# Kernel tuning notes

Hardware: AMD Instinct MI355X
Metric: run time of the kernel (lower is better)

Reference implementation:

```python
import jax, jax.numpy as jnp
import numpy as np
from jax import lax


def _lstm_layer(x, h0, c0, W_ih, W_hh, b_ih, b_hh):
    # x: [B,T,I]; precompute input projection for all timesteps: [B,T,4H]
    xg = jnp.einsum('bti,gi->btg', x, W_ih) + b_ih

    def step(carry, xg_t):
        h, c = carry
        gates = xg_t + h @ W_hh.T + b_hh  # [B,4H]
        i, f, g, o = jnp.split(gates, 4, axis=-1)  # PyTorch LSTMCell gate order
        i = jax.nn.sigmoid(i)
        f = jax.nn.sigmoid(f)
        g = jnp.tanh(g)
        o = jax.nn.sigmoid(o)
        c = f * c + i * g
        h = o * jnp.tanh(c)
        return (h, c), h

    (h, c), ys = lax.scan(step, (h0, c0), jnp.swapaxes(xg, 0, 1))  # scan over T
    return jnp.swapaxes(ys, 0, 1), h, c  # [B,T,H], [B,H], [B,H]


def setup_inputs() -> dict:
    key = jax.random.key(0)
    ks = jax.random.split(key, 10)
    B, T, I, H = 128, 256, 256, 1024
    s = 0.02
    return {
        'x': jax.random.normal(ks[0], (B, T, I), jnp.float32),
        'hx0': jnp.zeros((2, B, H), jnp.float32),
        'cx0': jnp.zeros((2, B, H), jnp.float32),
        'W_ih0': jax.random.normal(ks[1], (4 * H, I), jnp.float32) * s,
        'W_hh0': jax.random.normal(ks[2], (4 * H, H), jnp.float32) * s,
        'b_ih0': jax.random.normal(ks[3], (4 * H,), jnp.float32) * s,
        'b_hh0': jax.random.normal(ks[4], (4 * H,), jnp.float32) * s,
        'W_ih1': jax.random.normal(ks[5], (4 * H, H), jnp.float32) * s,
        'W_hh1': jax.random.normal(ks[6], (4 * H, H), jnp.float32) * s,
        'b_ih1': jax.random.normal(ks[7], (4 * H,), jnp.float32) * s,
        'b_hh1': jax.random.normal(ks[8], (4 * H,), jnp.float32) * s,
    }


def reference(x, hx0, cx0, W_ih0, W_hh0, b_ih0, b_hh0, W_ih1, W_hh1, b_ih1, b_hh1):
    # Eval mode / variational_inference=False with dropout=0.0: masks are exact ones.
    x, h, c = _lstm_layer(x, hx0[0], cx0[0], W_ih0, W_hh0, b_ih0, b_hh0)
    x, h, c = _lstm_layer(x, hx0[1], cx0[1], W_ih1, W_hh1, b_ih1, b_hh1)
    return x, h, c
```

## Files before the change

### kernel.cpp

```cpp
#include <hip/hip_runtime.h>

typedef __attribute__((ext_vector_type(8))) short short8;
typedef __attribute__((ext_vector_type(4))) float f32x4;

#define DEV static __device__ __forceinline__

DEV unsigned short f2b(float f) {
    union { float f; unsigned u; } v; v.f = f;
    unsigned r = (v.u + 0x7FFFu + ((v.u >> 16) & 1u)) >> 16;
    return (unsigned short)r;
}
DEV float b2f(unsigned short s) {
    union { unsigned u; float f; } v; v.u = ((unsigned)s) << 16;
    return v.f;
}
DEV float sigm(float x) { return 1.0f / (1.0f + __expf(-x)); }


__global__ void k_f2b(const float* __restrict__ src, unsigned short* __restrict__ dst, int n4) {
    int i = blockIdx.x * blockDim.x + threadIdx.x;
    if (i < n4) {
        float4 v = ((const float4*)src)[i];
        ushort4 o;
        o.x = f2b(v.x); o.y = f2b(v.y); o.z = f2b(v.z); o.w = f2b(v.w);
        ((ushort4*)dst)[i] = o;
    }
}

__global__ void k_perm(const float* __restrict__ src, unsigned short* __restrict__ dst, int Kq) {
    int i = blockIdx.x * blockDim.x + threadIdx.x;
    int total = 4096 * Kq;
    if (i >= total) return;
    int rp = i / Kq, kq = i - rp * Kq;
    int j = rp >> 2, g = rp & 3;
    float4 v = ((const float4*)src)[(size_t)(g * 1024 + j) * Kq + kq];
    ushort4 o;
    o.x = f2b(v.x); o.y = f2b(v.y); o.z = f2b(v.z); o.w = f2b(v.w);
    ((ushort4*)dst)[(size_t)rp * Kq + kq] = o;
}

__global__ void k_bias(const float* __restrict__ bi0, const float* __restrict__ bh0,
                       const float* __restrict__ bi1, const float* __restrict__ bh1,
                       float* __restrict__ d0, float* __restrict__ d1) {
    int i = blockIdx.x * blockDim.x + threadIdx.x;
    if (i < 4096) {
        int j = i >> 2, g = i & 3, s = g * 1024 + j;
        d0[i] = bi0[s] + bh0[s];
        d1[i] = bi1[s] + bh1[s];
    }
}

__global__ void k_init(const float* __restrict__ hx, const float* __restrict__ cx,
                       unsigned* __restrict__ hB0, unsigned* __restrict__ hB1,
                       float* __restrict__ c0, float* __restrict__ c1) {
    int i = blockIdx.x * blockDim.x + threadIdx.x;
    if (i < 128 * 512) {
        int b = i >> 9, j = i & 511;
        const float* p0 = hx + (size_t)b * 1024 + j * 2;
        const float* p1 = hx + 131072 + (size_t)b * 1024 + j * 2;
        hB0[i] = (unsigned)f2b(p0[0]) | ((unsigned)f2b(p0[1]) << 16);
        hB1[i] = (unsigned)f2b(p1[0]) | ((unsigned)f2b(p1[1]) << 16);
        c0[i * 2] = cx[i * 2];
        c0[i * 2 + 1] = cx[i * 2 + 1];
        c1[i * 2] = cx[131072 + i * 2];
        c1[i * 2 + 1] = cx[131072 + i * 2 + 1];
    }
}

__global__ __launch_bounds__(256) void k_gemm(
    const unsigned short* __restrict__ A, const unsigned short* __restrict__ W,
    unsigned short* __restrict__ out, int K, int t0, int TC) {
    __shared__ unsigned short ldsA[128 * 40];
    __shared__ unsigned short ldsB[128 * 40];
    const int tid = threadIdx.x;
    const int w = tid >> 6, l = tid & 63;
    const int wm = w >> 1, wn = w & 1;
    const int bm = blockIdx.x, bn = blockIdx.y;
    const int lr = l & 15, lk = (l >> 4) * 8;

    const int row0 = tid >> 2, inb = (tid & 3) << 4;
    const int row1 = row0 + 64;
    const int v0 = bm * 128 + row0, v1 = bm * 128 + row1;
    const size_t ar0 = (size_t)((v0 / TC) * 256 + t0 + (v0 % TC));
    const size_t ar1 = (size_t)((v1 / TC) * 256 + t0 + (v1 % TC));
    const size_t br0 = (size_t)(bn * 128 + row0);
    const size_t br1 = (size_t)(bn * 128 + row1);

    f32x4 acc[4][4];
#pragma unroll
    for (int a = 0; a < 4; a++)
#pragma unroll
        for (int b = 0; b < 4; b++) acc[a][b] = (f32x4){0.f, 0.f, 0.f, 0.f};

    for (int ks = 0; ks < K; ks += 32) {
        uint4 a0 = *(const uint4*)((const char*)A + (ar0 * K + ks) * 2 + inb);
        uint4 a1 = *(const uint4*)((const char*)A + (ar1 * K + ks) * 2 + inb);
        uint4 b0 = *(const uint4*)((const char*)W + (br0 * K + ks) * 2 + inb);
        uint4 b1 = *(const uint4*)((const char*)W + (br1 * K + ks) * 2 + inb);
        *(uint4*)((char*)ldsA + row0 * 80 + inb) = a0;
        *(uint4*)((char*)ldsA + row1 * 80 + inb) = a1;
        *(uint4*)((char*)ldsB + row0 * 80 + inb) = b0;
        *(uint4*)((char*)ldsB + row1 * 80 + inb) = b1;
        __syncthreads();
        short8 af[4], bf[4];
#pragma unroll
        for (int mt = 0; mt < 4; mt++)
            af[mt] = *(const short8*)((const char*)ldsA + (wm * 64 + mt * 16 + lr) * 80 + lk * 2);
#pragma unroll
        for (int nt = 0; nt < 4; nt++)
            bf[nt] = *(const short8*)((const char*)ldsB + (wn * 64 + nt * 16 + lr) * 80 + lk * 2);
#pragma unroll
        for (int mt = 0; mt < 4; mt++)
#pragma unroll
            for (int nt = 0; nt < 4; nt++)
                acc[mt][nt] = __builtin_amdgcn_mfma_f32_16x16x32_bf16(af[mt], bf[nt], acc[mt][nt], 0, 0, 0);
        __syncthreads();
    }

#pragma unroll
    for (int mt = 0; mt < 4; mt++)
#pragma unroll
        for (int nt = 0; nt < 4; nt++)
#pragma unroll
            for (int v4 = 0; v4 < 4; v4++) {
                int vr = bm * 128 + wm * 64 + mt * 16 + (l >> 4) * 4 + v4;
                int col = bn * 128 + wn * 64 + nt * 16 + lr;
                out[(size_t)vr * 4096 + col] = f2b(acc[mt][nt][v4]);
            }
}

template<int LAYER>
__global__ __launch_bounds__(512, 2) void k_lstm(
    const unsigned short* __restrict__ Wh,
    const unsigned short* __restrict__ xg,
    const float* __restrict__ bias,
    float* __restrict__ cbuf,
    unsigned* __restrict__ hA,
    unsigned* __restrict__ hB,
    unsigned short* __restrict__ y0,
    float* __restrict__ out,
    unsigned* __restrict__ cnt,
    int t0, int TC)
{
    extern __shared__ char smem[];
    unsigned short* ldsW = (unsigned short*)smem;
    float* P0 = (float*)(smem + 64 * 2064);
    float* P1 = P0 + 16 * 132;
    float* P2 = P1 + 16 * 132;

    const int tid = threadIdx.x;
    const int g  = (int)blockIdx.x >> 5;
    const int nb = (int)blockIdx.x & 31;
    const int w  = tid >> 6;
    const int l  = tid & 63;
    const int lr = l & 15, lq = l >> 4;

    {
        const char* src = (const char*)(Wh + (size_t)nb * 128 * 1024);
#pragma unroll
        for (int it = 0; it < 16; it++) {
            int idx = it * 512 + tid;
            int row = idx >> 7, inr = (idx & 127) << 4;
            *(uint4*)(smem + row * 2064 + inr) = *(const uint4*)(src + (size_t)row * 2048 + inr);
        }
    }
    short8 wreg[16];
    {
        const unsigned short* src = Wh + (size_t)(nb * 128 + 64) * 1024 + w * 128;
#pragma unroll
        for (int ct = 0; ct < 4; ct++)
#pragma unroll
            for (int kk = 0; kk < 4; kk++)
                wreg[ct * 4 + kk] =
                    *(const short8*)(src + (size_t)(ct * 16 + lr) * 1024 + kk * 32 + lq * 8);
    }

    const int er = tid >> 4, ep = tid & 15;
    const int eb = g * 16 + (er & 15);
    const int ec0 = nb * 128 + ep * 8;
    const int eu0 = nb * 32 + ep * 2;
    float2 c2 = make_float2(0.f, 0.f);
    float4 bsA = make_float4(0.f, 0.f, 0.f, 0.f);
    float4 bsB = make_float4(0.f, 0.f, 0.f, 0.f);
    if (tid < 256) {
        c2 = *(const float2*)(cbuf + (size_t)eb * 1024 + eu0);
        bsA = *(const float4*)(bias + ec0);
        bsB = *(const float4*)(bias + ec0 + 4);
    }

    const size_t abase = (size_t)(g * 16 + lr) * 256 + (size_t)w * 32 + lq * 2;
    const char* wp = (const char*)ldsW + (size_t)lr * 2064 + w * 256 + lq * 16;

    unsigned* cmy = cnt + g * 32;

    __syncthreads();

    for (int dt = 0; dt < TC; dt++) {
        const int t = t0 + dt;
        uint4 xv = make_uint4(0, 0, 0, 0);
        if (tid < 256)
            xv = *(const uint4*)(xg + (size_t)eb * ((size_t)TC * 4096) + (size_t)dt * 4096 + ec0);

        if (dt > 0) {
            unsigned tgt = 32u * (unsigned)dt;
            while (__hip_atomic_load(cmy, __ATOMIC_RELAXED, __HIP_MEMORY_SCOPE_AGENT) < tgt) {}
        }

        const unsigned long long* ap =
            (const unsigned long long*)((t & 1) ? hA : hB) + abase;
        f32x4 acc[8];
#pragma unroll
        for (int i = 0; i < 8; i++) acc[i] = (f32x4){0.f, 0.f, 0.f, 0.f};
#pragma unroll
        for (int kk = 0; kk < 4; kk++) {
            union { unsigned long long u[2]; short8 s; } av;
            av.u[0] = __hip_atomic_load(ap + kk * 8,     __ATOMIC_RELAXED, __HIP_MEMORY_SCOPE_AGENT);
            av.u[1] = __hip_atomic_load(ap + kk * 8 + 1, __ATOMIC_RELAXED, __HIP_MEMORY_SCOPE_AGENT);
#pragma unroll
            for (int ct = 0; ct < 4; ct++) {
                short8 b = *(const short8*)(wp + (size_t)ct * 16 * 2064 + kk * 64);
                acc[ct] = __builtin_amdgcn_mfma_f32_16x16x32_bf16(av.s, b, acc[ct], 0, 0, 0);
            }
#pragma unroll
            for (int ct = 0; ct < 4; ct++)
                acc[4 + ct] = __builtin_amdgcn_mfma_f32_16x16x32_bf16(av.s, wreg[ct * 4 + kk], acc[4 + ct], 0, 0, 0);
        }

        if (w >= 5) {
            float* P = (w == 5) ? P0 : (w == 6) ? P1 : P2;
#pragma unroll
            for (int i = 0; i < 8; i++)
#pragma unroll
                for (int v = 0; v < 4; v++)
                    P[(lq * 4 + v) * 132 + i * 16 + lr] = acc[i][v];
        }
        __syncthreads();
        if (w >= 2 && w <= 4) {
            float* P = (w == 2) ? P0 : (w == 3) ? P1 : P2;
#pragma unroll
            for (int i = 0; i < 8; i++)
#pragma unroll
                for (int v = 0; v < 4; v++)
                    P[(lq * 4 + v) * 132 + i * 16 + lr] += acc[i][v];
        }
        __syncthreads();
        if (w < 2) {
            float* P = (w == 0) ? P0 : P1;
#pragma unroll
            for (int i = 0; i < 8; i++)
#pragma unroll
                for (int v = 0; v < 4; v++)
                    P[(lq * 4 + v) * 132 + i * 16 + lr] += acc[i][v];
        }
        __syncthreads();

        float h0v = 0.f, h1v = 0.f;
        if (tid < 256) {
            const float* pa = P0 + er * 132 + ep * 8;
            const float* pb = P1 + er * 132 + ep * 8;
            const float* pc = P2 + er * 132 + ep * 8;
            const unsigned short* xs = (const unsigned short*)&xv;
            float p0 = pa[0] + pb[0] + pc[0] + b2f(xs[0]) + bsA.x;
            float p1 = pa[1] + pb[1] + pc[1] + b2f(xs[1]) + bsA.y;
            float p2 = pa[2] + pb[2] + pc[2] + b2f(xs[2]) + bsA.z;
            float p3 = pa[3] + pb[3] + pc[3] + b2f(xs[3]) + bsA.w;
            float q0 = pa[4] + pb[4] + pc[4] + b2f(xs[4]) + bsB.x;
            float q1 = pa[5] + pb[5] + pc[5] + b2f(xs[5]) + bsB.y;
            float q2 = pa[6] + pb[6] + pc[6] + b2f(xs[6]) + bsB.z;
            float q3 = pa[7] + pb[7] + pc[7] + b2f(xs[7]) + bsB.w;
            float i0 = sigm(p0), f0 = sigm(p1), gv0 = tanhf(p2), o0 = sigm(p3);
            float i1 = sigm(q0), f1 = sigm(q1), gv1 = tanhf(q2), o1 = sigm(q3);
            c2.x = f0 * c2.x + i0 * gv0;
            c2.y = f1 * c2.y + i1 * gv1;
            h0v = o0 * tanhf(c2.x);
            h1v = o1 * tanhf(c2.y);
            unsigned hp = (unsigned)f2b(h0v) | ((unsigned)f2b(h1v) << 16);
            unsigned* hout = (t & 1) ? hB : hA;
            __hip_atomic_store(hout + (size_t)eb * 512 + eu0 / 2, hp,
                               __ATOMIC_RELAXED, __HIP_MEMORY_SCOPE_AGENT);
        }
        __syncthreads();
        if (tid == 0)
            __hip_atomic_fetch_add(cmy, 1u, __ATOMIC_RELAXED, __HIP_MEMORY_SCOPE_AGENT);

        if (tid < 256) {
            if (LAYER == 0) {
                unsigned hp = (unsigned)f2b(h0v) | ((unsigned)f2b(h1v) << 16);
                ((unsigned*)y0)[((size_t)eb * 256 + t) * 512 + eu0 / 2] = hp;
            } else {
                *(float2*)(out + ((size_t)eb * 256 + t) * 1024 + eu0) = make_float2(h0v, h1v);
                if (t == 255) {
                    *(float2*)(out + (size_t)128 * 256 * 1024 + (size_t)eb * 1024 + eu0) =
                        make_float2(h0v, h1v);
                    *(float2*)(out + (size_t)128 * 256 * 1024 + (size_t)128 * 1024 + (size_t)eb * 1024 + eu0) =
                        make_float2(c2.x, c2.y);
                }
            }
        }
    }
    if (tid < 256)
        *(float2*)(cbuf + (size_t)eb * 1024 + eu0) = c2;
}


extern "C" void kernel_launch(void* const* d_in, const int* in_sizes, int n_in,
                              void* d_out, int out_size, void* d_ws, size_t ws_size,
                              hipStream_t stream) {
    const float* x    = (const float*)d_in[0];
    const float* hx0  = (const float*)d_in[1];
    const float* cx0  = (const float*)d_in[2];
    const float* Wih0 = (const float*)d_in[3];
    const float* Whh0 = (const float*)d_in[4];
    const float* bih0 = (const float*)d_in[5];
    const float* bhh0 = (const float*)d_in[6];
    const float* Wih1 = (const float*)d_in[7];
    const float* Whh1 = (const float*)d_in[8];
    const float* bih1 = (const float*)d_in[9];
    const float* bhh1 = (const float*)d_in[10];
    float* out = (float*)d_out;

    const int B = 128, T = 256, I = 256, H = 1024, G4 = 4096;
    const unsigned SMEM_BYTES = 64 * 2064 + 3 * 16 * 132 * 4;

    hipFuncSetAttribute((const void*)&k_lstm<0>, hipFuncAttributeMaxDynamicSharedMemorySize, SMEM_BYTES);
    hipFuncSetAttribute((const void*)&k_lstm<1>, hipFuncAttributeMaxDynamicSharedMemorySize, SMEM_BYTES);

    char* p = (char*)d_ws;
    auto alloc = [&](size_t bytes) { char* r = p; p += (bytes + 255) & ~(size_t)255; return r; };
    unsigned short* xbf   = (unsigned short*)alloc((size_t)B * T * I * 2);
    unsigned short* Wih0p = (unsigned short*)alloc((size_t)G4 * I * 2);
    unsigned short* Whh0p = (unsigned short*)alloc((size_t)G4 * H * 2);
    unsigned short* Wih1p = (unsigned short*)alloc((size_t)G4 * H * 2);
    unsigned short* Whh1p = (unsigned short*)alloc((size_t)G4 * H * 2);
    float* bias0 = (float*)alloc(G4 * 4);
    float* bias1 = (float*)alloc(G4 * 4);
    unsigned short* y0 = (unsigned short*)alloc((size_t)B * T * H * 2);
    unsigned* hA0 = (unsigned*)alloc((size_t)B * 512 * 4);
    unsigned* hB0 = (unsigned*)alloc((size_t)B * 512 * 4);
    unsigned* hA1 = (unsigned*)alloc((size_t)B * 512 * 4);
    unsigned* hB1 = (unsigned*)alloc((size_t)B * 512 * 4);
    float* c0 = (float*)alloc((size_t)B * H * 4);
    float* c1 = (float*)alloc((size_t)B * H * 4);
    unsigned* cnt = (unsigned*)alloc(8 * 128);
    size_t fixed = (size_t)(p - (char*)d_ws);
    int TC = 256;
    while (TC > 1 && fixed + (size_t)B * TC * G4 * 2 + 256 > ws_size) TC >>= 1;
    unsigned short* xg = (unsigned short*)alloc((size_t)B * TC * G4 * 2);

    k_f2b<<<(B * T * I / 4 + 255) / 256, 256, 0, stream>>>(x, xbf, B * T * I / 4);
    k_perm<<<(G4 * (I / 4) + 255) / 256, 256, 0, stream>>>(Wih0, Wih0p, I / 4);
    k_perm<<<(G4 * (H / 4) + 255) / 256, 256, 0, stream>>>(Whh0, Whh0p, H / 4);
    k_perm<<<(G4 * (H / 4) + 255) / 256, 256, 0, stream>>>(Wih1, Wih1p, H / 4);
    k_perm<<<(G4 * (H / 4) + 255) / 256, 256, 0, stream>>>(Whh1, Whh1p, H / 4);
    k_bias<<<16, 256, 0, stream>>>(bih0, bhh0, bih1, bhh1, bias0, bias1);
    k_init<<<256, 256, 0, stream>>>(hx0, cx0, hB0, hB1, c0, c1);

    for (int t0 = 0; t0 < T; t0 += TC) {
        k_gemm<<<dim3(TC, 32), 256, 0, stream>>>(xbf, Wih0p, xg, I, t0, TC);
        hipMemsetAsync(cnt, 0, 8 * 128, stream);
        int t0v = t0, TCv = TC;
        const unsigned short* Whp = Whh0p;
        const unsigned short* xgp = xg;
        const float* bp = bias0;
        float* cp = c0;
        unsigned* ha = hA0; unsigned* hb = hB0;
        unsigned short* y0p = y0;
        float* op = nullptr;
        unsigned* cp2 = cnt;
        void* args[] = {&Whp, &xgp, &bp, &cp, &ha, &hb, &y0p, &op, &cp2, &t0v, &TCv};
        hipLaunchCooperativeKernel((const void*)&k_lstm<0>, dim3(256), dim3(512), args, SMEM_BYTES, stream);
    }
    for (int t0 = 0; t0 < T; t0 += TC) {
        k_gemm<<<dim3(TC, 32), 256, 0, stream>>>(y0, Wih1p, xg, H, t0, TC);
        hipMemsetAsync(cnt, 0, 8 * 128, stream);
        int t0v = t0, TCv = TC;
        const unsigned short* Whp = Whh1p;
        const unsigned short* xgp = xg;
        const float* bp = bias1;
        float* cp = c1;
        unsigned* ha = hA1; unsigned* hb = hB1;
        unsigned short* y0p = nullptr;
        float* op = out;
        unsigned* cp2 = cnt;
        void* args[] = {&Whp, &xgp, &bp, &cp, &ha, &hb, &y0p, &op, &cp2, &t0v, &TCv};
        hipLaunchCooperativeKernel((const void*)&k_lstm<1>, dim3(256), dim3(512), args, SMEM_BYTES, stream);
    }
}
```

Measured before the change: 3.091 ms.

## Replace shared atomic counter barrier with per-block step flags and targeted waits

Each block now publishes its completed timestep to its own padded flag slot with a plain atomic store, instead of all 32 blocks in a group doing fetch-add on one counter. Each wave polls only the four producer blocks whose h slice it consumes (lanes split across the flags, combined with __all), so it no longer waits on the whole group. The aim is to remove contention on a single counter and to let waves start as soon as their own inputs are ready. Flags are indexed by absolute t and reset once per launch, which removes the per-chunk memset. The cost is more polling loads per wave.

Measured after the change: 3.046 ms. About the same (-1.4%).

```diff
diff --git a/kernel.cpp b/kernel.cpp
--- a/kernel.cpp
+++ b/kernel.cpp
@@ -139,7 +139,7 @@
     unsigned* __restrict__ hB,
     unsigned short* __restrict__ y0,
     float* __restrict__ out,
-    unsigned* __restrict__ cnt,
+    unsigned* __restrict__ flags,
     int t0, int TC)
 {
     extern __shared__ char smem[];
@@ -191,7 +191,8 @@
     const size_t abase = (size_t)(g * 16 + lr) * 256 + (size_t)w * 32 + lq * 2;
     const char* wp = (const char*)ldsW + (size_t)lr * 2064 + w * 256 + lq * 16;
 
-    unsigned* cmy = cnt + g * 32;
+    const unsigned* fpw = flags + (size_t)(g * 32 + w * 4 + (l & 3)) * 16;
+    unsigned* fmine = flags + (size_t)(g * 32 + nb) * 16;
 
     __syncthreads();
 
@@ -201,9 +202,10 @@
         if (tid < 256)
             xv = *(const uint4*)(xg + (size_t)eb * ((size_t)TC * 4096) + (size_t)dt * 4096 + ec0);
 
-        if (dt > 0) {
-            unsigned tgt = 32u * (unsigned)dt;
-            while (__hip_atomic_load(cmy, __ATOMIC_RELAXED, __HIP_MEMORY_SCOPE_AGENT) < tgt) {}
+        if (t > 0) {
+            const unsigned tgt = (unsigned)t;
+            while (!__all(__hip_atomic_load(fpw, __ATOMIC_RELAXED,
+                                            __HIP_MEMORY_SCOPE_AGENT) >= tgt)) {}
         }
 
         const unsigned long long* ap =
@@ -281,7 +283,8 @@
         }
         __syncthreads();
         if (tid == 0)
-            __hip_atomic_fetch_add(cmy, 1u, __ATOMIC_RELAXED, __HIP_MEMORY_SCOPE_AGENT);
+            __hip_atomic_store(fmine, (unsigned)(t + 1),
+                               __ATOMIC_RELAXED, __HIP_MEMORY_SCOPE_AGENT);
 
         if (tid < 256) {
             if (LAYER == 0) {
@@ -321,6 +324,7 @@
 
     const int B = 128, T = 256, I = 256, H = 1024, G4 = 4096;
     const unsigned SMEM_BYTES = 64 * 2064 + 3 * 16 * 132 * 4;
+    const int FLAGS_U32 = 8 * 32 * 16;
 
     hipFuncSetAttribute((const void*)&k_lstm<0>, hipFuncAttributeMaxDynamicSharedMemorySize, SMEM_BYTES);
     hipFuncSetAttribute((const void*)&k_lstm<1>, hipFuncAttributeMaxDynamicSharedMemorySize, SMEM_BYTES);
@@ -341,12 +345,14 @@
     unsigned* hB1 = (unsigned*)alloc((size_t)B * 512 * 4);
     float* c0 = (float*)alloc((size_t)B * H * 4);
     float* c1 = (float*)alloc((size_t)B * H * 4);
-    unsigned* cnt = (unsigned*)alloc(8 * 128);
+    unsigned* flags0 = (unsigned*)alloc((size_t)2 * FLAGS_U32 * 4);
+    unsigned* flags1 = flags0 + FLAGS_U32;
     size_t fixed = (size_t)(p - (char*)d_ws);
     int TC = 256;
     while (TC > 1 && fixed + (size_t)B * TC * G4 * 2 + 256 > ws_size) TC >>= 1;
     unsigned short* xg = (unsigned short*)alloc((size_t)B * TC * G4 * 2);
 
+    hipMemsetAsync(flags0, 0, (size_t)2 * FLAGS_U32 * 4, stream);
     k_f2b<<<(B * T * I / 4 + 255) / 256, 256, 0, stream>>>(x, xbf, B * T * I / 4);
     k_perm<<<(G4 * (I / 4) + 255) / 256, 256, 0, stream>>>(Wih0, Wih0p, I / 4);
     k_perm<<<(G4 * (H / 4) + 255) / 256, 256, 0, stream>>>(Whh0, Whh0p, H / 4);
@@ -357,7 +363,6 @@
 
     for (int t0 = 0; t0 < T; t0 += TC) {
         k_gemm<<<dim3(TC, 32), 256, 0, stream>>>(xbf, Wih0p, xg, I, t0, TC);
-        hipMemsetAsync(cnt, 0, 8 * 128, stream);
         int t0v = t0, TCv = TC;
         const unsigned short* Whp = Whh0p;
         const unsigned short* xgp = xg;
@@ -366,13 +371,12 @@
         unsigned* ha = hA0; unsigned* hb = hB0;
         unsigned short* y0p = y0;
         float* op = nullptr;
-        unsigned* cp2 = cnt;
-        void* args[] = {&Whp, &xgp, &bp, &cp, &ha, &hb, &y0p, &op, &cp2, &t0v, &TCv};
+        unsigned* fl = flags0;
+        void* args[] = {&Whp, &xgp, &bp, &cp, &ha, &hb, &y0p, &op, &fl, &t0v, &TCv};
         hipLaunchCooperativeKernel((const void*)&k_lstm<0>, dim3(256), dim3(512), args, SMEM_BYTES, stream);
     }
     for (int t0 = 0; t0 < T; t0 += TC) {
         k_gemm<<<dim3(TC, 32), 256, 0, stream>>>(y0, Wih1p, xg, H, t0, TC);
-        hipMemsetAsync(cnt, 0, 8 * 128, stream);
         int t0v = t0, TCv = TC;
         const unsigned short* Whp = Whh1p;
         const unsigned short* xgp = xg;
@@ -381,8 +385,8 @@
         unsigned* ha = hA1; unsigned* hb = hB1;
         unsigned short* y0p = nullptr;
         float* op = out;
-        unsigned* cp2 = cnt;
-        void* args[] = {&Whp, &xgp, &bp, &cp, &ha, &hb, &y0p, &op, &cp2, &t0v, &TCv};
+        unsigned* fl = flags1;
+        void* args[] = {&Whp, &xgp, &bp, &cp, &ha, &hb, &y0p, &op, &fl, &t0v, &TCv};
         hipLaunchCooperativeKernel((const void*)&k_lstm<1>, dim3(256), dim3(512), args, SMEM_BYTES, stream);
     }
 }
```
